# Kernel optimization log

Hardware: AMD Instinct MI355X
Metric: run time of the kernel (lower is better)

## Reference

```python
import jax, jax.numpy as jnp
import numpy as np

NUM_HEADS = 8
B, L, D = 4, 1024, 512


def sinusoidal_embeddings(length, dim, decay_term=10000.0):
    positions = jnp.arange(1 - length, length, dtype=jnp.float32).reshape(-1, 1)
    div_term = jnp.exp(-jnp.arange(0, dim, 2, dtype=jnp.float32) * (np.log(decay_term) / dim))
    return jnp.concatenate([jnp.sin(positions * div_term), jnp.cos(positions * div_term)], axis=1)


def setup_inputs() -> dict:
    key = jax.random.key(0)
    k1, k2 = jax.random.split(key)
    x = jax.random.normal(k1, (B, L, D), dtype=jnp.float32)
    W = jax.random.normal(k2, (D, 3 * D), dtype=jnp.float32) * 0.02
    b = jnp.zeros((3 * D,), dtype=jnp.float32)
    return {"x": x, "W": W, "b": b}


def reference(x, W, b):
    batch, length, dim = x.shape
    d_head = dim // NUM_HEADS
    # pointwise Conv(3*dim, kernel_size=1) == dense projection
    proj = jnp.einsum('bld,de->ble', x, W) + b  # [B, L, 3*dim]
    # split heads exactly as the module: reshape to [B,L,H,3*d_head], move heads, split into q,k,v
    proj = proj.reshape(batch, length, NUM_HEADS, 3 * d_head).transpose(0, 2, 1, 3)
    q, k, v = jnp.split(proj, 3, axis=3)  # each [B, H, L, d_head]
    qk = jnp.einsum('bhqd,bhkd->bhqk', q, k)
    # relative position scores via gather (unoptimized path)
    emb_matrix = sinusoidal_embeddings(length, d_head)  # [2L-1, d_head]
    indices = jnp.arange(length)[:, None] - jnp.arange(length) + length - 1  # [L, L]
    embeddings = emb_matrix[indices]  # [L, L, d_head]
    qe = jnp.einsum('bhqd,qkd->bhqk', q, embeddings)
    weights = jax.nn.softmax((qk + qe) / jnp.sqrt(jnp.float32(d_head)), axis=-1)
    output = jnp.einsum('bhqk,bhkd->bhqd', weights, v)
    return output.transpose(0, 2, 1, 3).reshape(batch, length, dim)
```

## Files before the change

### kernel.cpp

```cpp
#include <hip/hip_runtime.h>

typedef unsigned short UST;
typedef __attribute__((ext_vector_type(8))) __bf16 bf16x8;
typedef __attribute__((ext_vector_type(4))) float f32x4;
typedef __attribute__((ext_vector_type(16))) float f32x16;

#define NB 4
#define NH 8
#define LSEQ 1024
#define DMODEL 512
#define DH 64

__device__ __forceinline__ UST f2bf(float f) {
  union { float f; unsigned u; } v; v.f = f;
  unsigned u = v.u;
  return (UST)((u + 0x7FFFu + ((u >> 16) & 1u)) >> 16);
}
__device__ __forceinline__ float bf2f(UST h) {
  union { unsigned u; float f; } v; v.u = ((unsigned)h) << 16;
  return v.f;
}
__device__ __forceinline__ unsigned cvt_pk_bf16(float lo, float hi) {
  unsigned r;
  asm volatile("v_cvt_pk_bf16_f32 %0, %1, %2" : "=v"(r) : "v"(lo), "v"(hi));
  return r;
}

__global__ void k_convert_x(const float* __restrict__ x, UST* __restrict__ xbf) {
  int i = blockIdx.x * 256 + threadIdx.x;
  float4 v = ((const float4*)x)[i];
  ushort4 o;
  o.x = f2bf(v.x); o.y = f2bf(v.y); o.z = f2bf(v.z); o.w = f2bf(v.w);
  ((ushort4*)xbf)[i] = o;
}

__global__ void k_transpose_W(const float* __restrict__ W, UST* __restrict__ WT) {
  __shared__ float tile[64][65];
  int n0 = blockIdx.x * 64;
  int k0 = blockIdx.y * 64;
  int tx = threadIdx.x & 63, ty = threadIdx.x >> 6;
#pragma unroll
  for (int i = 0; i < 16; ++i) {
    int k = ty + i * 4;
    tile[k][tx] = W[(size_t)(k0 + k) * 1536 + n0 + tx];
  }
  __syncthreads();
#pragma unroll
  for (int i = 0; i < 16; ++i) {
    int n = ty + i * 4;
    WT[(size_t)(n0 + n) * 512 + k0 + tx] = f2bf(tile[tx][n]);
  }
}

__global__ __launch_bounds__(256) void k_proj(
    const UST* __restrict__ xbf, const UST* __restrict__ WT, const float* __restrict__ bias,
    UST* __restrict__ qext, UST* __restrict__ kext, UST* __restrict__ vT) {
  int m0 = blockIdx.x * 128;
  int n0 = blockIdx.y * 64;
  int t = threadIdx.x;
  int lane = t & 63, w = t >> 6;
  int wr = w >> 1, wc = w & 1;
  int g = lane >> 4, c16 = lane & 15;

  __shared__ UST AtS[128 * 64];
  __shared__ UST BtS[64 * 64];

  const char* Ag = (const char*)(xbf + (size_t)m0 * 512);
  const char* Bg = (const char*)(WT + (size_t)n0 * 512);

  bf16x8 areg[4], breg[2];
#pragma unroll
  for (int c = 0; c < 4; ++c) {
    int u = c * 256 + t, r = u >> 3, s = u & 7;
    areg[c] = *(const bf16x8*)(Ag + (size_t)r * 1024 + s * 16);
  }
#pragma unroll
  for (int c = 0; c < 2; ++c) {
    int u = c * 256 + t, r = u >> 3, s = u & 7;
    breg[c] = *(const bf16x8*)(Bg + (size_t)r * 1024 + s * 16);
  }

  f32x4 acc[4][2] = {};
  for (int kk = 0; kk < 512; kk += 64) {
    __syncthreads();
#pragma unroll
    for (int c = 0; c < 4; ++c) {
      int u = c * 256 + t, r = u >> 3, s = u & 7;
      *(bf16x8*)((char*)AtS + (size_t)r * 128 + (s ^ (r & 7)) * 16) = areg[c];
    }
#pragma unroll
    for (int c = 0; c < 2; ++c) {
      int u = c * 256 + t, r = u >> 3, s = u & 7;
      *(bf16x8*)((char*)BtS + (size_t)r * 128 + (s ^ (r & 7)) * 16) = breg[c];
    }
    __syncthreads();

    if (kk + 64 < 512) {
      size_t cb = (size_t)(kk + 64) * 2;
#pragma unroll
      for (int c = 0; c < 4; ++c) {
        int u = c * 256 + t, r = u >> 3, s = u & 7;
        areg[c] = *(const bf16x8*)(Ag + (size_t)r * 1024 + cb + s * 16);
      }
#pragma unroll
      for (int c = 0; c < 2; ++c) {
        int u = c * 256 + t, r = u >> 3, s = u & 7;
        breg[c] = *(const bf16x8*)(Bg + (size_t)r * 1024 + cb + s * 16);
      }
    }

#pragma unroll
    for (int kf = 0; kf < 2; ++kf) {
      bf16x8 af[4], bfr[2];
#pragma unroll
      for (int rf = 0; rf < 4; ++rf) {
        int r = wr * 64 + rf * 16 + c16;
        int s = (kf * 4 + g) ^ (r & 7);
        af[rf] = *(const bf16x8*)((const char*)AtS + (size_t)r * 128 + s * 16);
      }
#pragma unroll
      for (int cf = 0; cf < 2; ++cf) {
        int r = wc * 32 + cf * 16 + c16;
        int s = (kf * 4 + g) ^ (r & 7);
        bfr[cf] = *(const bf16x8*)((const char*)BtS + (size_t)r * 128 + s * 16);
      }
      __builtin_amdgcn_s_setprio(1);
#pragma unroll
      for (int rf = 0; rf < 4; ++rf)
#pragma unroll
        for (int cf = 0; cf < 2; ++cf)
          acc[rf][cf] = __builtin_amdgcn_mfma_f32_16x16x32_bf16(af[rf], bfr[cf], acc[rf][cf], 0, 0, 0);
      __builtin_amdgcn_s_setprio(0);
    }
  }

#pragma unroll
  for (int rf = 0; rf < 4; ++rf) {
#pragma unroll
    for (int cf = 0; cf < 2; ++cf) {
      int c = n0 + wc * 32 + cf * 16 + c16;
      int h = c / 192, rem = c % 192;
      float bv = bias[c];
#pragma unroll
      for (int r = 0; r < 4; ++r) {
        int row = m0 + wr * 64 + rf * 16 + g * 4 + r;
        int bidx = row >> 10, ltok = row & 1023;
        int bh = bidx * 8 + h;
        float val = acc[rf][cf][r] + bv;
        if (rem < 64)
          qext[((size_t)bh * 1024 + ltok) * 128 + rem] = f2bf(val * 0.125f);
        else if (rem < 128)
          kext[((size_t)bh * 1024 + ltok) * 128 + (rem - 64)] = f2bf(val);
        else
          vT[((size_t)bh * 64 + (rem - 128)) * 1024 + ltok] = f2bf(val);
      }
    }
  }
}

__global__ void k_relpos(UST* __restrict__ qext, UST* __restrict__ kext) {
  int gid = blockIdx.x * 256 + threadIdx.x;
  int j = gid & 31;
  int l = (gid >> 5) & 1023;
  int bh = gid >> 15;
  float dd = exp2f((float)(-2 * j) * 0.20762050593046f);
  float ang = (float)l * dd;
  float s = __sinf(ang), c = __cosf(ang);
  UST* qp = qext + ((size_t)bh * 1024 + l) * 128;
  float qs = bf2f(qp[j]), qc = bf2f(qp[32 + j]);
  qp[64 + j] = f2bf(qs * s + qc * c);
  qp[96 + j] = f2bf(qc * s - qs * c);
  UST* kp = kext + ((size_t)bh * 1024 + l) * 128;
  kp[64 + j] = f2bf(c);
  kp[96 + j] = f2bf(s);
}

__global__ __launch_bounds__(256) void k_attn(
    const UST* __restrict__ qext, const UST* __restrict__ kext,
    const UST* __restrict__ vT, float* __restrict__ out) {
  int blk = ((blockIdx.x & 7) << 6) | (blockIdx.x >> 3);
  int qt = blk & 15, bh = blk >> 4;
  int b = bh >> 3, h = bh & 7;
  int q0 = qt * 64;
  int t = threadIdx.x;
  int lane = t & 63, w = t >> 6;
  int l31 = lane & 31, lh = lane >> 5;
  int wq = w >> 1, wk = w & 1;

  __shared__ UST KtS[64 * 128];
  __shared__ UST VtS[64 * 64];
  __shared__ float Lsum[2][2][32];

  const UST* qbase = qext + ((size_t)bh * 1024 + q0 + wq * 32 + l31) * 128 + lh * 8;
  bf16x8 qf[8];
#pragma unroll
  for (int c = 0; c < 8; ++c) qf[c] = *(const bf16x8*)&qbase[c * 16];

  const char* kgbase = (const char*)(kext + (size_t)bh * 1024 * 128);
  const char* vgbase = (const char*)(vT + (size_t)bh * 64 * 1024);

  f32x16 O[2] = {};
  float l_lane = 0.f;

  bf16x8 kreg[4], vreg[2];
  {
    const char* kg = kgbase;
#pragma unroll
    for (int c = 0; c < 4; ++c) {
      int u = c * 256 + t;
      kreg[c] = *(const bf16x8*)(kg + (size_t)(u >> 4) * 256 + (u & 15) * 16);
    }
    const char* vg = vgbase;
#pragma unroll
    for (int c = 0; c < 2; ++c) {
      int u = c * 256 + t;
      vreg[c] = *(const bf16x8*)(vg + (size_t)(u >> 3) * 2048 + (u & 7) * 16);
    }
  }

  int krow = wk * 32 + l31;
  int ksalt = (krow ^ (krow >> 3)) & 7;

  for (int k0 = 0; k0 < LSEQ; k0 += 64) {
    __syncthreads();
#pragma unroll
    for (int c = 0; c < 4; ++c) {
      int u = c * 256 + t, r = u >> 4, s = u & 15;
      *(bf16x8*)((char*)KtS + (size_t)r * 256 + (s ^ ((r ^ (r >> 3)) & 7)) * 16) = kreg[c];
    }
#pragma unroll
    for (int c = 0; c < 2; ++c) {
      int u = c * 256 + t, r = u >> 3, s = u & 7;
      *(bf16x8*)((char*)VtS + (size_t)r * 128 + (s ^ ((r ^ (r >> 3)) & 7)) * 16) = vreg[c];
    }
    __syncthreads();

    if (k0 + 64 < LSEQ) {
      const char* kg = kgbase + (size_t)(k0 + 64) * 256;
#pragma unroll
      for (int c = 0; c < 4; ++c) {
        int u = c * 256 + t;
        kreg[c] = *(const bf16x8*)(kg + (size_t)(u >> 4) * 256 + (u & 15) * 16);
      }
      const char* vg = vgbase + (size_t)(k0 + 64) * 2;
#pragma unroll
      for (int c = 0; c < 2; ++c) {
        int u = c * 256 + t;
        vreg[c] = *(const bf16x8*)(vg + (size_t)(u >> 3) * 2048 + (u & 7) * 16);
      }
    }

    f32x16 sa = {};
#pragma unroll
    for (int kh = 0; kh < 2; ++kh) {
      bf16x8 kfr[4];
#pragma unroll
      for (int kc = 0; kc < 4; ++kc) {
        int slot = ((kh * 4 + kc) * 2 + lh) ^ ksalt;
        kfr[kc] = *(const bf16x8*)((const char*)KtS + (size_t)krow * 256 + slot * 16);
      }
      __builtin_amdgcn_s_setprio(1);
#pragma unroll
      for (int kc = 0; kc < 4; ++kc)
        sa = __builtin_amdgcn_mfma_f32_32x32x16_bf16(kfr[kc], qf[kh * 4 + kc], sa, 0, 0, 0);
      __builtin_amdgcn_s_setprio(0);
    }

    float p[16];
#pragma unroll
    for (int i = 0; i < 16; ++i) {
      p[i] = __expf(sa[i]);
      l_lane += p[i];
    }
    unsigned wv[8], xv[8];
#pragma unroll
    for (int j = 0; j < 8; ++j) wv[j] = cvt_pk_bf16(p[2 * j], p[2 * j + 1]);
#pragma unroll
    for (int j = 0; j < 8; ++j) xv[j] = (unsigned)__shfl_xor((int)wv[j], 32, 64);
    int4 pa0i = lh ? (int4){(int)xv[2], (int)xv[3], (int)wv[2], (int)wv[3]}
                   : (int4){(int)wv[0], (int)wv[1], (int)xv[0], (int)xv[1]};
    int4 pa1i = lh ? (int4){(int)xv[6], (int)xv[7], (int)wv[6], (int)wv[7]}
                   : (int4){(int)wv[4], (int)wv[5], (int)xv[4], (int)xv[5]};
    bf16x8 pa[2] = {*(bf16x8*)&pa0i, *(bf16x8*)&pa1i};

#pragma unroll
    for (int dn = 0; dn < 2; ++dn) {
      int d = dn * 32 + l31;
      int dsalt = (d ^ (d >> 3)) & 7;
      bf16x8 vf[2];
#pragma unroll
      for (int kc = 0; kc < 2; ++kc) {
        int slot = (wk * 4 + kc * 2 + lh) ^ dsalt;
        vf[kc] = *(const bf16x8*)((const char*)VtS + (size_t)d * 128 + slot * 16);
      }
      __builtin_amdgcn_s_setprio(1);
#pragma unroll
      for (int kc = 0; kc < 2; ++kc)
        O[dn] = __builtin_amdgcn_mfma_f32_32x32x16_bf16(pa[kc], vf[kc], O[dn], 0, 0, 0);
      __builtin_amdgcn_s_setprio(0);
    }
  }

  l_lane += __shfl_xor(l_lane, 32, 64);
  if (lh == 0) Lsum[wk][wq][l31] = l_lane;
  __syncthreads();
  float* scratch = (float*)KtS;
  if (wk == 1) {
#pragma unroll
    for (int i = 0; i < 16; ++i) {
      int qr = wq * 32 + ((i & 3) + 8 * (i >> 2) + 4 * lh);
      scratch[qr * 64 + l31] = O[0][i];
      scratch[qr * 64 + 32 + l31] = O[1][i];
    }
  }
  __syncthreads();
  if (wk == 0) {
#pragma unroll
    for (int i = 0; i < 16; ++i) {
      int cr = (i & 3) + 8 * (i >> 2) + 4 * lh;
      int qr = wq * 32 + cr;
      float inv = 1.0f / (Lsum[0][wq][cr] + Lsum[1][wq][cr]);
      float* op = out + ((size_t)b * 1024 + q0 + qr) * 512 + h * 64;
      op[l31] = (O[0][i] + scratch[qr * 64 + l31]) * inv;
      op[32 + l31] = (O[1][i] + scratch[qr * 64 + 32 + l31]) * inv;
    }
  }
}

extern "C" void kernel_launch(void* const* d_in, const int* in_sizes, int n_in,
                              void* d_out, int out_size, void* d_ws, size_t ws_size,
                              hipStream_t stream) {
  const float* x = (const float*)d_in[0];
  const float* W = (const float*)d_in[1];
  const float* bias = (const float*)d_in[2];
  float* out = (float*)d_out;

  UST* ws = (UST*)d_ws;
  UST* xbf  = ws;
  UST* WT   = xbf + 4096 * 512;
  UST* qext = WT + 1536 * 512;
  UST* kext = qext + 32 * 1024 * 128;
  UST* vT   = kext + 32 * 1024 * 128;

  k_convert_x<<<dim3(2048), dim3(256), 0, stream>>>(x, xbf);
  k_transpose_W<<<dim3(24, 8), dim3(256), 0, stream>>>(W, WT);
  k_proj<<<dim3(32, 24), dim3(256), 0, stream>>>(xbf, WT, bias, qext, kext, vT);
  k_relpos<<<dim3(4096), dim3(256), 0, stream>>>(qext, kext);
  k_attn<<<dim3(512), dim3(256), 0, stream>>>(qext, kext, vT, out);
}
```

Before: 58.66 us.

## Double-buffer K/V tiles in LDS to cut one barrier per iteration

The K and V shared-memory tiles become two ping-pong buffers. Each iteration computes on the current buffer, then writes the prefetched registers into the other buffer and issues global loads two tiles ahead, so only one __syncthreads per iteration remains instead of two. This doubles LDS use (about 48KB), which may reduce occupancy, and moves the LDS stores after the compute. The barrier before the epilogue's reuse of KtS as scratch is removed, relying on the loop's trailing barrier.

```diff
diff --git a/kernel.cpp b/kernel.cpp
--- a/kernel.cpp
+++ b/kernel.cpp
@@ -187,8 +187,8 @@
   int l31 = lane & 31, lh = lane >> 5;
   int wq = w >> 1, wk = w & 1;
 
-  __shared__ UST KtS[64 * 128];
-  __shared__ UST VtS[64 * 64];
+  __shared__ UST KtS[2][64 * 128];
+  __shared__ UST VtS[2][64 * 64];
   __shared__ float Lsum[2][2][32];
 
   const UST* qbase = qext + ((size_t)bh * 1024 + q0 + wq * 32 + l31) * 128 + lh * 8;
@@ -203,52 +203,45 @@
   float l_lane = 0.f;
 
   bf16x8 kreg[4], vreg[2];
-  {
-    const char* kg = kgbase;
-#pragma unroll
-    for (int c = 0; c < 4; ++c) {
-      int u = c * 256 + t;
-      kreg[c] = *(const bf16x8*)(kg + (size_t)(u >> 4) * 256 + (u & 15) * 16);
-    }
-    const char* vg = vgbase;
-#pragma unroll
-    for (int c = 0; c < 2; ++c) {
-      int u = c * 256 + t;
-      vreg[c] = *(const bf16x8*)(vg + (size_t)(u >> 3) * 2048 + (u & 7) * 16);
-    }
-  }
+#pragma unroll
+  for (int c = 0; c < 4; ++c) {
+    int u = c * 256 + t;
+    kreg[c] = *(const bf16x8*)(kgbase + (size_t)(u >> 4) * 256 + (u & 15) * 16);
+  }
+#pragma unroll
+  for (int c = 0; c < 2; ++c) {
+    int u = c * 256 + t;
+    vreg[c] = *(const bf16x8*)(vgbase + (size_t)(u >> 3) * 2048 + (u & 7) * 16);
+  }
+#pragma unroll
+  for (int c = 0; c < 4; ++c) {
+    int u = c * 256 + t, r = u >> 4, s = u & 15;
+    *(bf16x8*)((char*)KtS[0] + (size_t)r * 256 + (s ^ ((r ^ (r >> 3)) & 7)) * 16) = kreg[c];
+  }
+#pragma unroll
+  for (int c = 0; c < 2; ++c) {
+    int u = c * 256 + t, r = u >> 3, s = u & 7;
+    *(bf16x8*)((char*)VtS[0] + (size_t)r * 128 + (s ^ ((r ^ (r >> 3)) & 7)) * 16) = vreg[c];
+  }
+#pragma unroll
+  for (int c = 0; c < 4; ++c) {
+    int u = c * 256 + t;
+    kreg[c] = *(const bf16x8*)(kgbase + 64 * 256 + (size_t)(u >> 4) * 256 + (u & 15) * 16);
+  }
+#pragma unroll
+  for (int c = 0; c < 2; ++c) {
+    int u = c * 256 + t;
+    vreg[c] = *(const bf16x8*)(vgbase + 64 * 2 + (size_t)(u >> 3) * 2048 + (u & 7) * 16);
+  }
+  __syncthreads();
 
   int krow = wk * 32 + l31;
   int ksalt = (krow ^ (krow >> 3)) & 7;
 
-  for (int k0 = 0; k0 < LSEQ; k0 += 64) {
-    __syncthreads();
-#pragma unroll
-    for (int c = 0; c < 4; ++c) {
-      int u = c * 256 + t, r = u >> 4, s = u & 15;
-      *(bf16x8*)((char*)KtS + (size_t)r * 256 + (s ^ ((r ^ (r >> 3)) & 7)) * 16) = kreg[c];
-    }
-#pragma unroll
-    for (int c = 0; c < 2; ++c) {
-      int u = c * 256 + t, r = u >> 3, s = u & 7;
-      *(bf16x8*)((char*)VtS + (size_t)r * 128 + (s ^ ((r ^ (r >> 3)) & 7)) * 16) = vreg[c];
-    }
-    __syncthreads();
-
-    if (k0 + 64 < LSEQ) {
-      const char* kg = kgbase + (size_t)(k0 + 64) * 256;
-#pragma unroll
-      for (int c = 0; c < 4; ++c) {
-        int u = c * 256 + t;
-        kreg[c] = *(const bf16x8*)(kg + (size_t)(u >> 4) * 256 + (u & 15) * 16);
-      }
-      const char* vg = vgbase + (size_t)(k0 + 64) * 2;
-#pragma unroll
-      for (int c = 0; c < 2; ++c) {
-        int u = c * 256 + t;
-        vreg[c] = *(const bf16x8*)(vg + (size_t)(u >> 3) * 2048 + (u & 7) * 16);
-      }
-    }
+  for (int it = 0; it < 16; ++it) {
+    int cur = it & 1;
+    const char* Kb = (const char*)(KtS[cur]);
+    const char* Vb = (const char*)(VtS[cur]);
 
     f32x16 sa = {};
 #pragma unroll
@@ -257,7 +250,7 @@
 #pragma unroll
       for (int kc = 0; kc < 4; ++kc) {
         int slot = ((kh * 4 + kc) * 2 + lh) ^ ksalt;
-        kfr[kc] = *(const bf16x8*)((const char*)KtS + (size_t)krow * 256 + slot * 16);
+        kfr[kc] = *(const bf16x8*)(Kb + (size_t)krow * 256 + slot * 16);
       }
       __builtin_amdgcn_s_setprio(1);
 #pragma unroll
@@ -291,7 +284,7 @@
 #pragma unroll
       for (int kc = 0; kc < 2; ++kc) {
         int slot = (wk * 4 + kc * 2 + lh) ^ dsalt;
-        vf[kc] = *(const bf16x8*)((const char*)VtS + (size_t)d * 128 + slot * 16);
+        vf[kc] = *(const bf16x8*)(Vb + (size_t)d * 128 + slot * 16);
       }
       __builtin_amdgcn_s_setprio(1);
 #pragma unroll
@@ -299,12 +292,41 @@
         O[dn] = __builtin_amdgcn_mfma_f32_32x32x16_bf16(pa[kc], vf[kc], O[dn], 0, 0, 0);
       __builtin_amdgcn_s_setprio(0);
     }
+
+    if (it < 15) {
+      char* Kw = (char*)(KtS[cur ^ 1]);
+      char* Vw = (char*)(VtS[cur ^ 1]);
+#pragma unroll
+      for (int c = 0; c < 4; ++c) {
+        int u = c * 256 + t, r = u >> 4, s = u & 15;
+        *(bf16x8*)(Kw + (size_t)r * 256 + (s ^ ((r ^ (r >> 3)) & 7)) * 16) = kreg[c];
+      }
+#pragma unroll
+      for (int c = 0; c < 2; ++c) {
+        int u = c * 256 + t, r = u >> 3, s = u & 7;
+        *(bf16x8*)(Vw + (size_t)r * 128 + (s ^ ((r ^ (r >> 3)) & 7)) * 16) = vreg[c];
+      }
+      if (it < 14) {
+        const char* kg = kgbase + (size_t)(it + 2) * 64 * 256;
+#pragma unroll
+        for (int c = 0; c < 4; ++c) {
+          int u = c * 256 + t;
+          kreg[c] = *(const bf16x8*)(kg + (size_t)(u >> 4) * 256 + (u & 15) * 16);
+        }
+        const char* vg = vgbase + (size_t)(it + 2) * 64 * 2;
+#pragma unroll
+        for (int c = 0; c < 2; ++c) {
+          int u = c * 256 + t;
+          vreg[c] = *(const bf16x8*)(vg + (size_t)(u >> 3) * 2048 + (u & 7) * 16);
+        }
+      }
+    }
+    __syncthreads();
   }
 
   l_lane += __shfl_xor(l_lane, 32, 64);
   if (lh == 0) Lsum[wk][wq][l31] = l_lane;
-  __syncthreads();
-  float* scratch = (float*)KtS;
+  float* scratch = (float*)KtS[0];
   if (wk == 1) {
 #pragma unroll
     for (int i = 0; i < 16; ++i) {
```

After: 58.05 us. No clear change (-1.0%).
